# Kernel optimization log

Hardware: AMD Instinct MI355X
Metric: run time of the kernel (lower is better)

The kernel has to match this reference:

```python
import jax, jax.numpy as jnp
import numpy as np

B, V = 256, 128000

def setup_inputs() -> dict:
    key = jax.random.key(0)
    k1, k2 = jax.random.split(key)
    logits = jax.random.normal(k1, (B, V), dtype=jnp.float32)
    # temperatures in [0.5, 1.5) to avoid degenerate near-zero temps
    temperatures = jax.random.uniform(k2, (B,), dtype=jnp.float32, minval=0.5, maxval=1.5)
    return {"logits": logits, "temperatures": temperatures, "top_k": 50}

def reference(logits, temperatures, top_k):
    # temperature scale (logits.float().div_(temps[:, None]))
    scaled = logits.astype(jnp.float32) / temperatures[:, None]          # [B, V]
    # top-k threshold: k-th largest value per row
    kth = jax.lax.top_k(scaled, top_k)[0][:, -1:]                        # [B, 1]
    # mask everything strictly below the k-th value to -inf
    masked = jnp.where(scaled < kth, -jnp.inf, scaled)                   # [B, V]
    # softmax + multinomial(1)  ==  categorical over masked logits
    samples = jax.random.categorical(jax.random.key(42), masked, axis=-1)  # [B]
    return samples
```

## Files before the change

### kernel.cpp

```cpp
#include <hip/hip_runtime.h>

#define THREADS 1024
#define BINS 4096
#define CAP 4096
#define FLOOR_KEY 0xC0200000u
#define MARGIN 8u

__device__ __forceinline__ unsigned rotl32(unsigned x, unsigned r) {
  return (x << r) | (x >> (32u - r));
}

__device__ __forceinline__ unsigned threefry_xor_0_42(unsigned x0, unsigned x1) {
  const unsigned k0 = 0u, k1 = 42u, k2 = 0u ^ 42u ^ 0x1BD11BDAu;
  x0 += k0; x1 += k1;
#define TF_R(r) { x0 += x1; x1 = rotl32(x1, r); x1 ^= x0; }
  TF_R(13) TF_R(15) TF_R(26) TF_R(6)
  x0 += k1; x1 += k2 + 1u;
  TF_R(17) TF_R(29) TF_R(16) TF_R(24)
  x0 += k2; x1 += k0 + 2u;
  TF_R(13) TF_R(15) TF_R(26) TF_R(6)
  x0 += k0; x1 += k1 + 3u;
  TF_R(17) TF_R(29) TF_R(16) TF_R(24)
  x0 += k1; x1 += k2 + 4u;
  TF_R(13) TF_R(15) TF_R(26) TF_R(6)
  x0 += k2; x1 += k0 + 5u;
#undef TF_R
  return x0 ^ x1;
}

__device__ __forceinline__ float gumbel_at(unsigned flat) {
  unsigned bits = threefry_xor_0_42(0u, flat);
  float fl = __uint_as_float((bits >> 9) | 0x3F800000u) - 1.0f;
  const float tiny = 1.17549435e-38f;
  float u = fmaxf(fl + tiny, tiny);
  return -logf(-logf(u));
}

__device__ __forceinline__ unsigned f2k(float f) {
  unsigned b = __float_as_uint(f);
  return (b & 0x80000000u) ? ~b : (b ^ 0x80000000u);
}
__device__ __forceinline__ float k2f(unsigned k) {
  unsigned b = (k & 0x80000000u) ? (k ^ 0x80000000u) : ~k;
  return __uint_as_float(b);
}

__global__ __launch_bounds__(THREADS) void sampler_kernel(
    const float* __restrict__ logits, const float* __restrict__ temps,
    const int* __restrict__ topk_ptr, int* __restrict__ out, int V) {
  const int row = blockIdx.x;
  const int tid = threadIdx.x;
  const unsigned K = (unsigned)(*topk_ptr);

  const float* rowp = logits + (size_t)row * (size_t)V;
  const float4* rowp4 = (const float4*)rowp;
  const int nv4 = V >> 2;
  const int half4 = nv4 >> 1;

  __shared__ unsigned hist[BINS];
  __shared__ unsigned cand_key[CAP];
  __shared__ unsigned cand_idx[CAP];
  __shared__ float    rv[THREADS];
  __shared__ unsigned ri[THREADS];
  __shared__ unsigned ncand, sBstar, sAbove, sK50;

  if (tid == 0) { ncand = 0u; sBstar = 0u; sAbove = 0u; sK50 = 0u; }
  __syncthreads();

  for (int i = tid; i < half4; i += THREADS) {
    float4 a = rowp4[i];
    float4 b = rowp4[i + half4];
    float f[8] = {a.x, a.y, a.z, a.w, b.x, b.y, b.z, b.w};
#pragma unroll
    for (int e = 0; e < 8; ++e) {
      unsigned key = f2k(f[e]);
      if (key >= FLOOR_KEY) {
        unsigned col = (unsigned)((e < 4 ? i : i + half4) * 4 + (e & 3));
        unsigned p = atomicAdd(&ncand, 1u);
        if (p < CAP) { cand_key[p] = key; cand_idx[p] = col; }
      }
    }
  }
  for (int j = (half4 * 2) * 4 + tid; j < V; j += THREADS) {
    unsigned key = f2k(rowp[j]);
    if (key >= FLOOR_KEY) {
      unsigned p = atomicAdd(&ncand, 1u);
      if (p < CAP) { cand_key[p] = key; cand_idx[p] = (unsigned)j; }
    }
  }
  __syncthreads();

  const bool tryFast = (ncand >= K && ncand <= (unsigned)CAP);
  unsigned c = min(ncand, (unsigned)CAP);

  if (tryFast) {
    for (unsigned i = tid; i < c; i += THREADS) {
      unsigned ki = cand_key[i];
      unsigned gt = 0, eq = 0;
      for (unsigned j = 0; j < c; ++j) {
        unsigned kj = cand_key[j];
        gt += (kj > ki) ? 1u : 0u;
        eq += (kj == ki) ? 1u : 0u;
      }
      if (gt < K && gt + eq >= K) sK50 = ki;
    }
  }
  __syncthreads();

  const bool fastOK = tryFast && (sK50 >= FLOOR_KEY + MARGIN);

  float bestV = -INFINITY;
  unsigned bestI = 0xFFFFFFFFu;
  const float t = temps[row];
  const unsigned rowBase = (unsigned)row * (unsigned)V;

  if (!fastOK) {
    for (int i = tid; i < BINS; i += THREADS) hist[i] = 0u;
    if (tid == 0) ncand = 0u;
    __syncthreads();

    for (int i = tid; i < nv4; i += THREADS) {
      float4 v = rowp4[i];
      atomicAdd(&hist[f2k(v.x) >> 20], 1u);
      atomicAdd(&hist[f2k(v.y) >> 20], 1u);
      atomicAdd(&hist[f2k(v.z) >> 20], 1u);
      atomicAdd(&hist[f2k(v.w) >> 20], 1u);
    }
    for (int j = nv4 * 4 + tid; j < V; j += THREADS) atomicAdd(&hist[f2k(rowp[j]) >> 20], 1u);
    __syncthreads();

    if (tid < 64) {
      const int lane = tid;
      unsigned s = 0;
      for (int k = 0; k < 64; ++k) s += hist[lane * 64 + k];
      unsigned suf = s;
#pragma unroll
      for (int off = 1; off < 64; off <<= 1) {
        unsigned o = __shfl_down(suf, off);
        if (lane + off < 64) suf += o;
      }
      unsigned sufn = __shfl_down(suf, 1);
      if (lane == 63) sufn = 0u;
      if (suf >= K && sufn < K) {
        unsigned run = sufn;
        for (int k = 63; k >= 0; --k) {
          unsigned h = hist[lane * 64 + k];
          unsigned nr = run + h;
          if (run < K && nr >= K) { sBstar = (unsigned)(lane * 64 + k); sAbove = run; }
          run = nr;
        }
      }
    }
    __syncthreads();

    const unsigned Bstar = sBstar;
    const unsigned cntAbove = sAbove;
    const unsigned long long binCeilP1 = ((unsigned long long)(Bstar + 1u)) << 20;
    const unsigned lowKey = (Bstar >= 1u) ? ((Bstar - 1u) << 20) : 0u;

    for (int i = tid; i < nv4; i += THREADS) {
      float4 v = rowp4[i];
      float f[4] = {v.x, v.y, v.z, v.w};
#pragma unroll
      for (int e = 0; e < 4; ++e) {
        unsigned key = f2k(f[e]);
        if (key < lowKey) continue;
        unsigned col = (unsigned)(i * 4 + e);
        if ((unsigned long long)key >= binCeilP1) {
          float sj = f[e] / t;
          float val = sj + gumbel_at(rowBase + col);
          if (val > bestV || (val == bestV && col < bestI)) { bestV = val; bestI = col; }
        } else {
          unsigned p = atomicAdd(&ncand, 1u);
          if (p < CAP) { cand_key[p] = key; cand_idx[p] = col; }
        }
      }
    }
    for (int j = nv4 * 4 + tid; j < V; j += THREADS) {
      unsigned key = f2k(rowp[j]);
      if (key < lowKey) continue;
      if ((unsigned long long)key >= binCeilP1) {
        float sj = rowp[j] / t;
        float val = sj + gumbel_at(rowBase + (unsigned)j);
        if (val > bestV || (val == bestV && (unsigned)j < bestI)) { bestV = val; bestI = (unsigned)j; }
      } else {
        unsigned p = atomicAdd(&ncand, 1u);
        if (p < CAP) { cand_key[p] = key; cand_idx[p] = (unsigned)j; }
      }
    }
    __syncthreads();

    c = min(ncand, (unsigned)CAP);
    for (unsigned i = tid; i < c; i += THREADS) {
      unsigned ki = cand_key[i];
      unsigned gt = 0, eq = 0;
      for (unsigned j = 0; j < c; ++j) {
        unsigned kj = cand_key[j];
        gt += (kj > ki) ? 1u : 0u;
        eq += (kj == ki) ? 1u : 0u;
      }
      if (cntAbove + gt < K && cntAbove + gt + eq >= K) sK50 = ki;
    }
    __syncthreads();
  }

  const float s50 = k2f(sK50) / t;
  for (unsigned i = tid; i < c; i += THREADS) {
    unsigned col = cand_idx[i];
    if (col >= (unsigned)V) continue;
    float sj = k2f(cand_key[i]) / t;
    if (sj >= s50) {
      float val = sj + gumbel_at(rowBase + col);
      if (val > bestV || (val == bestV && col < bestI)) { bestV = val; bestI = col; }
    }
  }

  rv[tid] = bestV; ri[tid] = bestI;
  __syncthreads();
  for (int off = THREADS / 2; off > 0; off >>= 1) {
    if (tid < off) {
      float v2 = rv[tid + off]; unsigned i2 = ri[tid + off];
      if (v2 > rv[tid] || (v2 == rv[tid] && i2 < ri[tid])) { rv[tid] = v2; ri[tid] = i2; }
    }
    __syncthreads();
  }
  if (tid == 0) out[row] = (int)((ri[0] < (unsigned)V) ? ri[0] : 0u);
}

extern "C" void kernel_launch(void* const* d_in, const int* in_sizes, int n_in,
                              void* d_out, int out_size, void* d_ws, size_t ws_size,
                              hipStream_t stream) {
  const float* logits = (const float*)d_in[0];
  const float* temps  = (const float*)d_in[1];
  const int*   topk   = (const int*)d_in[2];
  int* out = (int*)d_out;

  const int B = in_sizes[1];
  const int V = in_sizes[0] / B;

  sampler_kernel<<<B, THREADS, 0, stream>>>(logits, temps, topk, out, V);
}
```

Baseline: 219.5 us.

## Split candidate scan across multiple blocks per row into separate kernel

```diff
diff --git a/kernel.cpp b/kernel.cpp
--- a/kernel.cpp
+++ b/kernel.cpp
@@ -1,8 +1,14 @@
 #include <hip/hip_runtime.h>
 
-#define THREADS 1024
+#define T1 256
+#define SPLIT 8
+#define LDSCAP 1024
+#define CAP_ROW 2048
+#define OVF_BUMP (1u << 20)
+
+#define T2 1024
 #define BINS 4096
-#define CAP 4096
+#define CAPF 4096
 #define FLOOR_KEY 0xC0200000u
 #define MARGIN 8u
 
@@ -45,56 +51,101 @@
   return __uint_as_float(b);
 }
 
-__global__ __launch_bounds__(THREADS) void sampler_kernel(
+__global__ __launch_bounds__(T1) void scan_kernel(
+    const float* __restrict__ logits, unsigned* __restrict__ counters,
+    unsigned* __restrict__ okeys, unsigned* __restrict__ oidxs, int V) {
+  const int row = blockIdx.x / SPLIT;
+  const int chunk = blockIdx.x - row * SPLIT;
+  const int tid = threadIdx.x;
+  const int nv4 = V >> 2;
+  const int c4 = (nv4 + SPLIT - 1) / SPLIT;
+  const int beg = chunk * c4;
+  const int end = min(nv4, beg + c4);
+  const float* rowp = logits + (size_t)row * (size_t)V;
+  const float4* rowp4 = (const float4*)rowp;
+
+  __shared__ unsigned skey[LDSCAP];
+  __shared__ unsigned sidx[LDSCAP];
+  __shared__ unsigned snc, sbase;
+  if (tid == 0) snc = 0u;
+  __syncthreads();
+
+#pragma unroll 4
+  for (int i = beg + tid; i < end; i += T1) {
+    float4 v = rowp4[i];
+    float f[4] = {v.x, v.y, v.z, v.w};
+#pragma unroll
+    for (int e = 0; e < 4; ++e) {
+      unsigned key = f2k(f[e]);
+      if (key >= FLOOR_KEY) {
+        unsigned p = atomicAdd(&snc, 1u);
+        if (p < LDSCAP) { skey[p] = key; sidx[p] = (unsigned)(i * 4 + e); }
+      }
+    }
+  }
+  if (chunk == SPLIT - 1) {
+    for (int j = nv4 * 4 + tid; j < V; j += T1) {
+      unsigned key = f2k(rowp[j]);
+      if (key >= FLOOR_KEY) {
+        unsigned p = atomicAdd(&snc, 1u);
+        if (p < LDSCAP) { skey[p] = key; sidx[p] = (unsigned)j; }
+      }
+    }
+  }
+  __syncthreads();
+
+  const unsigned nc = snc;
+  const unsigned nb = min(nc, (unsigned)LDSCAP);
+  if (tid == 0) {
+    unsigned add = (nc > (unsigned)LDSCAP) ? (nb + OVF_BUMP) : nb;
+    sbase = atomicAdd(&counters[row], add);
+  }
+  __syncthreads();
+  const unsigned base = sbase;
+  unsigned* kout = okeys + (size_t)row * CAP_ROW;
+  unsigned* iout = oidxs + (size_t)row * CAP_ROW;
+  for (unsigned p = tid; p < nb; p += T1) {
+    unsigned g = base + p;
+    if (g < (unsigned)CAP_ROW) { kout[g] = skey[p]; iout[g] = sidx[p]; }
+  }
+}
+
+__global__ __launch_bounds__(T2) void select_kernel(
     const float* __restrict__ logits, const float* __restrict__ temps,
-    const int* __restrict__ topk_ptr, int* __restrict__ out, int V) {
+    const int* __restrict__ topk_ptr, const unsigned* __restrict__ counters,
+    const unsigned* __restrict__ okeys, const unsigned* __restrict__ oidxs,
+    int* __restrict__ out, int V) {
   const int row = blockIdx.x;
   const int tid = threadIdx.x;
   const unsigned K = (unsigned)(*topk_ptr);
-
+  const float t = temps[row];
+  const unsigned rowBase = (unsigned)row * (unsigned)V;
   const float* rowp = logits + (size_t)row * (size_t)V;
   const float4* rowp4 = (const float4*)rowp;
   const int nv4 = V >> 2;
-  const int half4 = nv4 >> 1;
 
   __shared__ unsigned hist[BINS];
-  __shared__ unsigned cand_key[CAP];
-  __shared__ unsigned cand_idx[CAP];
-  __shared__ float    rv[THREADS];
-  __shared__ unsigned ri[THREADS];
+  __shared__ unsigned cand_key[CAPF];
+  __shared__ unsigned cand_idx[CAPF];
+  __shared__ float    rv[T2];
+  __shared__ unsigned ri[T2];
   __shared__ unsigned ncand, sBstar, sAbove, sK50;
 
   if (tid == 0) { ncand = 0u; sBstar = 0u; sAbove = 0u; sK50 = 0u; }
   __syncthreads();
 
-  for (int i = tid; i < half4; i += THREADS) {
-    float4 a = rowp4[i];
-    float4 b = rowp4[i + half4];
-    float f[8] = {a.x, a.y, a.z, a.w, b.x, b.y, b.z, b.w};
-#pragma unroll
-    for (int e = 0; e < 8; ++e) {
-      unsigned key = f2k(f[e]);
-      if (key >= FLOOR_KEY) {
-        unsigned col = (unsigned)((e < 4 ? i : i + half4) * 4 + (e & 3));
-        unsigned p = atomicAdd(&ncand, 1u);
-        if (p < CAP) { cand_key[p] = key; cand_idx[p] = col; }
-      }
-    }
-  }
-  for (int j = (half4 * 2) * 4 + tid; j < V; j += THREADS) {
-    unsigned key = f2k(rowp[j]);
-    if (key >= FLOOR_KEY) {
-      unsigned p = atomicAdd(&ncand, 1u);
-      if (p < CAP) { cand_key[p] = key; cand_idx[p] = (unsigned)j; }
-    }
-  }
-  __syncthreads();
-
-  const bool tryFast = (ncand >= K && ncand <= (unsigned)CAP);
-  unsigned c = min(ncand, (unsigned)CAP);
+  const unsigned cnt = counters[row];
+  const bool tryFast = (cnt >= K && cnt <= (unsigned)CAP_ROW);
+  unsigned c = 0;
+  unsigned cntAbove = 0;
 
   if (tryFast) {
-    for (unsigned i = tid; i < c; i += THREADS) {
+    c = cnt;
+    const unsigned* kin = okeys + (size_t)row * CAP_ROW;
+    const unsigned* iin = oidxs + (size_t)row * CAP_ROW;
+    for (unsigned i = tid; i < c; i += T2) { cand_key[i] = kin[i]; cand_idx[i] = iin[i]; }
+    __syncthreads();
+    for (unsigned i = tid; i < c; i += T2) {
       unsigned ki = cand_key[i];
       unsigned gt = 0, eq = 0;
       for (unsigned j = 0; j < c; ++j) {
@@ -104,29 +155,27 @@
       }
       if (gt < K && gt + eq >= K) sK50 = ki;
     }
-  }
-  __syncthreads();
+    __syncthreads();
+  }
 
   const bool fastOK = tryFast && (sK50 >= FLOOR_KEY + MARGIN);
 
   float bestV = -INFINITY;
   unsigned bestI = 0xFFFFFFFFu;
-  const float t = temps[row];
-  const unsigned rowBase = (unsigned)row * (unsigned)V;
 
   if (!fastOK) {
-    for (int i = tid; i < BINS; i += THREADS) hist[i] = 0u;
-    if (tid == 0) ncand = 0u;
-    __syncthreads();
-
-    for (int i = tid; i < nv4; i += THREADS) {
+    for (int i = tid; i < BINS; i += T2) hist[i] = 0u;
+    if (tid == 0) { ncand = 0u; sK50 = 0u; }
+    __syncthreads();
+
+    for (int i = tid; i < nv4; i += T2) {
       float4 v = rowp4[i];
       atomicAdd(&hist[f2k(v.x) >> 20], 1u);
       atomicAdd(&hist[f2k(v.y) >> 20], 1u);
       atomicAdd(&hist[f2k(v.z) >> 20], 1u);
       atomicAdd(&hist[f2k(v.w) >> 20], 1u);
     }
-    for (int j = nv4 * 4 + tid; j < V; j += THREADS) atomicAdd(&hist[f2k(rowp[j]) >> 20], 1u);
+    for (int j = nv4 * 4 + tid; j < V; j += T2) atomicAdd(&hist[f2k(rowp[j]) >> 20], 1u);
     __syncthreads();
 
     if (tid < 64) {
@@ -154,11 +203,11 @@
     __syncthreads();
 
     const unsigned Bstar = sBstar;
-    const unsigned cntAbove = sAbove;
+    cntAbove = sAbove;
     const unsigned long long binCeilP1 = ((unsigned long long)(Bstar + 1u)) << 20;
     const unsigned lowKey = (Bstar >= 1u) ? ((Bstar - 1u) << 20) : 0u;
 
-    for (int i = tid; i < nv4; i += THREADS) {
+    for (int i = tid; i < nv4; i += T2) {
       float4 v = rowp4[i];
       float f[4] = {v.x, v.y, v.z, v.w};
 #pragma unroll
@@ -172,11 +221,11 @@
           if (val > bestV || (val == bestV && col < bestI)) { bestV = val; bestI = col; }
         } else {
           unsigned p = atomicAdd(&ncand, 1u);
-          if (p < CAP) { cand_key[p] = key; cand_idx[p] = col; }
+          if (p < CAPF) { cand_key[p] = key; cand_idx[p] = col; }
         }
       }
     }
-    for (int j = nv4 * 4 + tid; j < V; j += THREADS) {
+    for (int j = nv4 * 4 + tid; j < V; j += T2) {
       unsigned key = f2k(rowp[j]);
       if (key < lowKey) continue;
       if ((unsigned long long)key >= binCeilP1) {
@@ -185,13 +234,13 @@
         if (val > bestV || (val == bestV && (unsigned)j < bestI)) { bestV = val; bestI = (unsigned)j; }
       } else {
         unsigned p = atomicAdd(&ncand, 1u);
-        if (p < CAP) { cand_key[p] = key; cand_idx[p] = (unsigned)j; }
-      }
-    }
-    __syncthreads();
-
-    c = min(ncand, (unsigned)CAP);
-    for (unsigned i = tid; i < c; i += THREADS) {
+        if (p < CAPF) { cand_key[p] = key; cand_idx[p] = (unsigned)j; }
+      }
+    }
+    __syncthreads();
+
+    c = min(ncand, (unsigned)CAPF);
+    for (unsigned i = tid; i < c; i += T2) {
       unsigned ki = cand_key[i];
       unsigned gt = 0, eq = 0;
       for (unsigned j = 0; j < c; ++j) {
@@ -205,7 +254,7 @@
   }
 
   const float s50 = k2f(sK50) / t;
-  for (unsigned i = tid; i < c; i += THREADS) {
+  for (unsigned i = tid; i < c; i += T2) {
     unsigned col = cand_idx[i];
     if (col >= (unsigned)V) continue;
     float sj = k2f(cand_key[i]) / t;
@@ -217,7 +266,7 @@
 
   rv[tid] = bestV; ri[tid] = bestI;
   __syncthreads();
-  for (int off = THREADS / 2; off > 0; off >>= 1) {
+  for (int off = T2 / 2; off > 0; off >>= 1) {
     if (tid < off) {
       float v2 = rv[tid + off]; unsigned i2 = ri[tid + off];
       if (v2 > rv[tid] || (v2 == rv[tid] && i2 < ri[tid])) { rv[tid] = v2; ri[tid] = i2; }
@@ -238,5 +287,11 @@
   const int B = in_sizes[1];
   const int V = in_sizes[0] / B;
 
-  sampler_kernel<<<B, THREADS, 0, stream>>>(logits, temps, topk, out, V);
-}
+  unsigned* counters = (unsigned*)d_ws;
+  unsigned* okeys = counters + B;
+  unsigned* oidxs = okeys + (size_t)B * CAP_ROW;
+
+  hipMemsetAsync(counters, 0, (size_t)B * sizeof(unsigned), stream);
+  scan_kernel<<<B * SPLIT, T1, 0, stream>>>(logits, counters, okeys, oidxs, V);
+  select_kernel<<<B, T2, 0, stream>>>(logits, temps, topk, counters, okeys, oidxs, out, V);
+}
```

New measurement: 227.4 us. +3.6%, slower.
